# Kernel tuning notes

Hardware: AMD Instinct MI355X
Metric: run time of the kernel (lower is better)

Reference implementation:

```python
import jax, jax.numpy as jnp
import numpy as np

NUM_NODES = 100000
NODE_FEAT_DIM = 512
EDGE_FEAT_DIM = 512
MEM_DIM = NODE_FEAT_DIM + EDGE_FEAT_DIM  # 1024
BATCH = 65536


def setup_inputs() -> dict:
    key = jax.random.key(0)
    k_ids, k_mem, k_emb, kq, ks, kk = jax.random.split(key, 6)
    scale = 1.0 / np.sqrt(MEM_DIM)
    inp = {
        "node_ids": jax.random.randint(k_ids, (BATCH,), 0, NUM_NODES, dtype=jnp.int64)
        if jax.config.jax_enable_x64 else
        jax.random.randint(k_ids, (BATCH,), 0, NUM_NODES, dtype=jnp.int32),
        # memory bank: (N, 1, D); randomized (instead of the zero init) so math is non-trivial
        "node_memories": jax.random.normal(k_mem, (NUM_NODES, 1, MEM_DIM), dtype=jnp.float32) * 0.02,
        "node_embedding": jax.random.normal(k_emb, (NUM_NODES, MEM_DIM), dtype=jnp.float32) * 0.02,
        "Wq": jax.random.normal(jax.random.fold_in(kq, 0), (MEM_DIM, NODE_FEAT_DIM), dtype=jnp.float32) * scale,
        "bq": jnp.zeros((NODE_FEAT_DIM,), dtype=jnp.float32),
        "Ws": jax.random.normal(jax.random.fold_in(ks, 0), (MEM_DIM, NODE_FEAT_DIM), dtype=jnp.float32) * scale,
        "bs": jnp.zeros((NODE_FEAT_DIM,), dtype=jnp.float32),
        "Wk": jax.random.normal(jax.random.fold_in(kk, 0), (MEM_DIM, NODE_FEAT_DIM), dtype=jnp.float32) * scale,
        "bk": jnp.zeros((NODE_FEAT_DIM,), dtype=jnp.float32),
    }
    return inp


def reference(node_ids, node_memories, node_embedding, Wq, bq, Ws, bs, Wk, bk):
    ids = node_ids.astype(jnp.int32)
    # torch.sum(node_memories[ids], dim=2): reduces feature dim -> (B, 1)
    mem_sum = jnp.sum(node_memories[ids], axis=2)          # (B, 1)
    x = mem_sum + node_embedding[ids]                      # broadcast -> (B, D)
    q = jax.nn.sigmoid(x @ Wq + bq)                        # (B, node_feat_dim)
    s = jax.nn.sigmoid(x @ Ws + bs)
    k = jax.nn.sigmoid(x @ Wk + bk)
    return (q, s, k)
```

## Files before the change

kernel.cpp:

```cpp
#include <hip/hip_runtime.h>
#include <hip/hip_bf16.h>
#include <stdint.h>

#define BATCH_N 65536
#define KDIM 1024
#define NTOT 1536

typedef __bf16 bf16x8 __attribute__((ext_vector_type(8)));
typedef float f32x4 __attribute__((ext_vector_type(4)));

__device__ __forceinline__ unsigned short f2bf(float f) {
    unsigned u = __builtin_bit_cast(unsigned, f);
    u += 0x7FFFu + ((u >> 16) & 1u);
    return (unsigned short)(u >> 16);
}

__global__ __launch_bounds__(256) void prep_kernel(
    const int* __restrict__ ids,
    const float* __restrict__ mem,
    const float* __restrict__ emb,
    unsigned short* __restrict__ x)
{
    const int b = blockIdx.x;
    const int t = threadIdx.x;
    const int id = ids[b];
    const float4* m4 = (const float4*)(mem + (size_t)id * KDIM);
    const float4* e4 = (const float4*)(emb + (size_t)id * KDIM);
    float4 v = m4[t];
    float s = v.x + v.y + v.z + v.w;
    #pragma unroll
    for (int off = 32; off >= 1; off >>= 1) s += __shfl_down(s, off, 64);
    __shared__ float wsum[4];
    const int lane = t & 63, w = t >> 6;
    if (lane == 0) wsum[w] = s;
    __syncthreads();
    const float tot = wsum[0] + wsum[1] + wsum[2] + wsum[3];
    float4 e = e4[t];
    ushort4 o;
    o.x = f2bf(tot + e.x);
    o.y = f2bf(tot + e.y);
    o.z = f2bf(tot + e.z);
    o.w = f2bf(tot + e.w);
    const int k   = t * 4;
    const int ksw = k ^ ((b & 7) << 3);
    *(ushort4*)(x + (size_t)b * KDIM + ksw) = o;
}

__global__ __launch_bounds__(256) void wconv_kernel(
    const float* __restrict__ Wq, const float* __restrict__ Ws,
    const float* __restrict__ Wk, unsigned short* __restrict__ wt)
{
    const int gt = blockIdx.x * 256 + threadIdx.x;
    const int n  = gt % NTOT;
    const int kb = (gt / NTOT) * 4;
    const float* W = (n < 512) ? Wq : ((n < 1024) ? Ws : Wk);
    const int nn = n & 511;
    ushort4 o;
    o.x = f2bf(W[(size_t)(kb + 0) * 512 + nn]);
    o.y = f2bf(W[(size_t)(kb + 1) * 512 + nn]);
    o.z = f2bf(W[(size_t)(kb + 2) * 512 + nn]);
    o.w = f2bf(W[(size_t)(kb + 3) * 512 + nn]);
    const int ksw = kb ^ ((n & 7) << 3);
    *(ushort4*)(wt + (size_t)n * KDIM + ksw) = o;
}

#define BM 128
#define BN 128
#define BK 64
#define MT 512
#define NT 12
#define NWG (MT * NT)

__global__ __launch_bounds__(256, 2) void gemm_kernel(
    const unsigned short* __restrict__ X,
    const unsigned short* __restrict__ Wt,
    const float* __restrict__ bq, const float* __restrict__ bs,
    const float* __restrict__ bk, float* __restrict__ out)
{
    __shared__ __align__(16) unsigned short lA[BM * BK];
    __shared__ __align__(16) unsigned short lB[BN * BK];

    const int tid  = threadIdx.x;
    const int xcd  = blockIdx.x & 7;
    const int idx  = blockIdx.x >> 3;
    const int wgid = xcd * (NWG / 8) + idx;
    const int nt   = wgid % NT;
    const int mt   = wgid / NT;
    const int m0   = mt * BM;
    const int n0   = nt * BN;
    const int wid  = tid >> 6;
    const int lane = tid & 63;
    const int wr   = wid >> 1, wc = wid & 1;

    f32x4 acc[4][4];
    #pragma unroll
    for (int i = 0; i < 4; i++)
        #pragma unroll
        for (int j = 0; j < 4; j++)
            acc[i][j] = f32x4{0.f, 0.f, 0.f, 0.f};

    const unsigned short* gA = X  + (size_t)(m0 + (tid >> 3)) * KDIM + (size_t)(tid & 7) * 8;
    const unsigned short* gB = Wt + (size_t)(n0 + (tid >> 3)) * KDIM + (size_t)(tid & 7) * 8;

    for (int ks = 0; ks < KDIM; ks += BK) {
        __syncthreads();
        #pragma unroll
        for (int i = 0; i < 4; i++) {
            __builtin_amdgcn_global_load_lds(
                (const __attribute__((address_space(1))) void*)(gA + (size_t)i * 32 * KDIM + ks),
                (__attribute__((address_space(3))) void*)(&lA[(i * 256 + (tid & 192)) * 8]),
                16, 0, 0);
        }
        #pragma unroll
        for (int i = 0; i < 4; i++) {
            __builtin_amdgcn_global_load_lds(
                (const __attribute__((address_space(1))) void*)(gB + (size_t)i * 32 * KDIM + ks),
                (__attribute__((address_space(3))) void*)(&lB[(i * 256 + (tid & 192)) * 8]),
                16, 0, 0);
        }
        __syncthreads();

        #pragma unroll
        for (int kk = 0; kk < 2; kk++) {
            const int r16  = lane & 15;
            const int kbyt = ((lane >> 4) << 4) + kk * 64;
            const int kswz = kbyt ^ ((r16 & 7) << 4);
            bf16x8 af[4], bfr[4];
            #pragma unroll
            for (int i = 0; i < 4; i++) {
                const int row = wr * 64 + i * 16 + r16;
                af[i] = *(const bf16x8*)((const char*)lA + row * 128 + kswz);
            }
            #pragma unroll
            for (int j = 0; j < 4; j++) {
                const int row = wc * 64 + j * 16 + r16;
                bfr[j] = *(const bf16x8*)((const char*)lB + row * 128 + kswz);
            }
            #pragma unroll
            for (int i = 0; i < 4; i++)
                #pragma unroll
                for (int j = 0; j < 4; j++)
                    acc[i][j] = __builtin_amdgcn_mfma_f32_16x16x32_bf16(
                        af[i], bfr[j], acc[i][j], 0, 0, 0);
        }
    }

    const float* bias = (n0 < 512) ? bq : ((n0 < 1024) ? bs : bk);
    float* obase = out + (size_t)(n0 >> 9) * ((size_t)BATCH_N * 512);
    const int nb = n0 & 511;
    #pragma unroll
    for (int j = 0; j < 4; j++) {
        const int col = nb + wc * 64 + j * 16 + (lane & 15);
        const float bv = bias[col];
        #pragma unroll
        for (int i = 0; i < 4; i++) {
            const int rbase = m0 + wr * 64 + i * 16 + ((lane >> 4) << 2);
            #pragma unroll
            for (int r = 0; r < 4; r++) {
                float v = acc[i][j][r] + bv;
                v = 1.0f / (1.0f + __expf(-v));
                __builtin_nontemporal_store(v, &obase[(size_t)(rbase + r) * 512 + col]);
            }
        }
    }
}

extern "C" void kernel_launch(void* const* d_in, const int* in_sizes, int n_in,
                              void* d_out, int out_size, void* d_ws, size_t ws_size,
                              hipStream_t stream) {
    const int*   ids = (const int*)d_in[0];
    const float* mem = (const float*)d_in[1];
    const float* emb = (const float*)d_in[2];
    const float* Wq  = (const float*)d_in[3];
    const float* bq  = (const float*)d_in[4];
    const float* Ws  = (const float*)d_in[5];
    const float* bs  = (const float*)d_in[6];
    const float* Wk  = (const float*)d_in[7];
    const float* bk  = (const float*)d_in[8];
    float* out = (float*)d_out;

    unsigned short* x  = (unsigned short*)d_ws;
    unsigned short* wt = x + (size_t)BATCH_N * KDIM;

    hipLaunchKernelGGL(wconv_kernel, dim3(NTOT), dim3(256), 0, stream, Wq, Ws, Wk, wt);
    hipLaunchKernelGGL(prep_kernel, dim3(BATCH_N), dim3(256), 0, stream, ids, mem, emb, x);
    hipLaunchKernelGGL(gemm_kernel, dim3(NWG), dim3(256), 0, stream,
                       x, wt, bq, bs, bk, out);
}
```

Before: 415.3 us.

## Triple-buffer GEMM LDS with 512-thread 128x256 tiles and interleaved prefetch

Makes the GEMM tile 128x256 and the workgroup 512 threads in a 2x4 wave grid, so each A tile is reused across twice as many output columns. It adds a three-stage LDS ring filled with global_load_lds, issuing the prefetch of tile k+2 in the same phases that run MFMAs on tile k. It uses raw s_barrier and vmcnt waits plus s_setprio around the MFMA blocks, aiming to hide global-load latency behind compute. LDS use rises to 144 KB per block, which likely allows only one block per CU despite the launch bound, and the hand-placed waitcnts are easy to get wrong.

Measured after the change: 468.9 us. 12.9% more time.

```diff
diff --git a/kernel.cpp b/kernel.cpp
--- a/kernel.cpp
+++ b/kernel.cpp
@@ -65,20 +65,22 @@
 }
 
 #define BM 128
-#define BN 128
+#define BN 256
 #define BK 64
-#define MT 512
-#define NT 12
+#define MT (BATCH_N / BM)
+#define NT (NTOT / BN)
 #define NWG (MT * NT)
 
-__global__ __launch_bounds__(256, 2) void gemm_kernel(
+#define BAR() asm volatile("s_barrier" ::: "memory")
+
+__global__ __launch_bounds__(512, 2) void gemm_kernel(
     const unsigned short* __restrict__ X,
     const unsigned short* __restrict__ Wt,
     const float* __restrict__ bq, const float* __restrict__ bs,
     const float* __restrict__ bk, float* __restrict__ out)
 {
-    __shared__ __align__(16) unsigned short lA[BM * BK];
-    __shared__ __align__(16) unsigned short lB[BN * BK];
+    __shared__ __align__(16) unsigned short sA[3][BM * BK];
+    __shared__ __align__(16) unsigned short sB[3][BN * BK];
 
     const int tid  = threadIdx.x;
     const int xcd  = blockIdx.x & 7;
@@ -90,7 +92,11 @@
     const int n0   = nt * BN;
     const int wid  = tid >> 6;
     const int lane = tid & 63;
-    const int wr   = wid >> 1, wc = wid & 1;
+    const int wm   = wid >> 2;
+    const int wn   = wid & 3;
+    const int r16  = lane & 15;
+    const int kb0  = (lane >> 4) << 4;
+    const int ksw  = (r16 & 7) << 4;
 
     f32x4 acc[4][4];
     #pragma unroll
@@ -99,62 +105,74 @@
         for (int j = 0; j < 4; j++)
             acc[i][j] = f32x4{0.f, 0.f, 0.f, 0.f};
 
-    const unsigned short* gA = X  + (size_t)(m0 + (tid >> 3)) * KDIM + (size_t)(tid & 7) * 8;
-    const unsigned short* gB = Wt + (size_t)(n0 + (tid >> 3)) * KDIM + (size_t)(tid & 7) * 8;
-
-    for (int ks = 0; ks < KDIM; ks += BK) {
-        __syncthreads();
-        #pragma unroll
-        for (int i = 0; i < 4; i++) {
-            __builtin_amdgcn_global_load_lds(
-                (const __attribute__((address_space(1))) void*)(gA + (size_t)i * 32 * KDIM + ks),
-                (__attribute__((address_space(3))) void*)(&lA[(i * 256 + (tid & 192)) * 8]),
-                16, 0, 0);
-        }
-        #pragma unroll
-        for (int i = 0; i < 4; i++) {
-            __builtin_amdgcn_global_load_lds(
-                (const __attribute__((address_space(1))) void*)(gB + (size_t)i * 32 * KDIM + ks),
-                (__attribute__((address_space(3))) void*)(&lB[(i * 256 + (tid & 192)) * 8]),
-                16, 0, 0);
-        }
-        __syncthreads();
-
-        #pragma unroll
-        for (int kk = 0; kk < 2; kk++) {
-            const int r16  = lane & 15;
-            const int kbyt = ((lane >> 4) << 4) + kk * 64;
-            const int kswz = kbyt ^ ((r16 & 7) << 4);
-            bf16x8 af[4], bfr[4];
-            #pragma unroll
-            for (int i = 0; i < 4; i++) {
-                const int row = wr * 64 + i * 16 + r16;
-                af[i] = *(const bf16x8*)((const char*)lA + row * 128 + kswz);
-            }
-            #pragma unroll
-            for (int j = 0; j < 4; j++) {
-                const int row = wc * 64 + j * 16 + r16;
-                bfr[j] = *(const bf16x8*)((const char*)lB + row * 128 + kswz);
-            }
-            #pragma unroll
-            for (int i = 0; i < 4; i++)
-                #pragma unroll
-                for (int j = 0; j < 4; j++)
-                    acc[i][j] = __builtin_amdgcn_mfma_f32_16x16x32_bf16(
-                        af[i], bfr[j], acc[i][j], 0, 0, 0);
-        }
+    const unsigned short* gA = X  + (size_t)(m0 + (tid >> 3)) * KDIM + (tid & 7) * 8;
+    const unsigned short* gB = Wt + (size_t)(n0 + (tid >> 3)) * KDIM + (tid & 7) * 8;
+    const int ldst = (tid & 448) * 8;
+
+#define STA(buf, kt, c) __builtin_amdgcn_global_load_lds( \
+    (const __attribute__((address_space(1))) void*)(gA + (size_t)(c) * 64 * KDIM + (kt) * BK), \
+    (__attribute__((address_space(3))) void*)(&sA[buf][(c) * 4096 + ldst]), 16, 0, 0)
+#define STB(buf, kt, c) __builtin_amdgcn_global_load_lds( \
+    (const __attribute__((address_space(1))) void*)(gB + (size_t)(c) * 64 * KDIM + (kt) * BK), \
+    (__attribute__((address_space(3))) void*)(&sB[buf][(c) * 4096 + ldst]), 16, 0, 0)
+
+#define PHASE(rb, kkc, STAGE_STMTS, VMW) do {                                   \
+    const char* pa = (const char*)&sA[rb][0];                                    \
+    const char* pb = (const char*)&sB[rb][0];                                    \
+    bf16x8 af[4], bfr[4];                                                        \
+    _Pragma("unroll")                                                            \
+    for (int i = 0; i < 4; i++)                                                  \
+        af[i] = *(const bf16x8*)(pa + (wm * 64 + i * 16 + r16) * 128             \
+                                    + ((kb0 + (kkc) * 64) ^ ksw));               \
+    _Pragma("unroll")                                                            \
+    for (int j = 0; j < 4; j++)                                                  \
+        bfr[j] = *(const bf16x8*)(pb + (wn * 64 + j * 16 + r16) * 128            \
+                                     + ((kb0 + (kkc) * 64) ^ ksw));              \
+    STAGE_STMTS;                                                                 \
+    BAR();                                                                       \
+    asm volatile("s_waitcnt lgkmcnt(0)" ::: "memory");                           \
+    __builtin_amdgcn_s_setprio(1);                                               \
+    _Pragma("unroll")                                                            \
+    for (int i = 0; i < 4; i++)                                                  \
+        _Pragma("unroll")                                                        \
+        for (int j = 0; j < 4; j++)                                              \
+            acc[i][j] = __builtin_amdgcn_mfma_f32_16x16x32_bf16(                 \
+                af[i], bfr[j], acc[i][j], 0, 0, 0);                              \
+    __builtin_amdgcn_s_setprio(0);                                               \
+    VMW;                                                                         \
+    BAR();                                                                       \
+} while (0)
+
+    STA(0, 0, 0); STA(0, 0, 1); STB(0, 0, 0); STB(0, 0, 1); STB(0, 0, 2); STB(0, 0, 3);
+    STA(1, 1, 0); STA(1, 1, 1); STB(1, 1, 0); STB(1, 1, 1); STB(1, 1, 2); STB(1, 1, 3);
+    asm volatile("s_waitcnt vmcnt(6)" ::: "memory");
+    BAR();
+
+    int rb = 0, wb = 2;
+    for (int k = 0; k < 14; ++k) {
+        const int kt = k + 2;
+        PHASE(rb, 0, ({ STA(wb, kt, 0); STA(wb, kt, 1); STB(wb, kt, 0); }), (void)0);
+        PHASE(rb, 1, ({ STB(wb, kt, 1); STB(wb, kt, 2); STB(wb, kt, 3); }),
+              asm volatile("s_waitcnt vmcnt(6)" ::: "memory"));
+        rb = (rb == 2) ? 0 : rb + 1;
+        wb = (wb == 2) ? 0 : wb + 1;
     }
-
-    const float* bias = (n0 < 512) ? bq : ((n0 < 1024) ? bs : bk);
-    float* obase = out + (size_t)(n0 >> 9) * ((size_t)BATCH_N * 512);
-    const int nb = n0 & 511;
+    PHASE(rb, 0, (void)0, (void)0);
+    PHASE(rb, 1, (void)0, asm volatile("s_waitcnt vmcnt(0)" ::: "memory"));
+    rb = (rb == 2) ? 0 : rb + 1;
+    PHASE(rb, 0, (void)0, (void)0);
+    PHASE(rb, 1, (void)0, (void)0);
+
+    const int grp = nt >> 1;
+    const float* bias = (grp == 0) ? bq : ((grp == 1) ? bs : bk);
+    float* obase = out + (size_t)grp * ((size_t)BATCH_N * 512);
     #pragma unroll
     for (int j = 0; j < 4; j++) {
-        const int col = nb + wc * 64 + j * 16 + (lane & 15);
+        const int col = (nt & 1) * 256 + wn * 64 + j * 16 + r16;
         const float bv = bias[col];
         #pragma unroll
         for (int i = 0; i < 4; i++) {
-            const int rbase = m0 + wr * 64 + i * 16 + ((lane >> 4) << 2);
+            const int rbase = m0 + wm * 64 + i * 16 + ((lane >> 4) << 2);
             #pragma unroll
             for (int r = 0; r < 4; r++) {
                 float v = acc[i][j][r] + bv;
@@ -163,6 +181,9 @@
             }
         }
     }
+#undef STA
+#undef STB
+#undef PHASE
 }
 
 extern "C" void kernel_launch(void* const* d_in, const int* in_sizes, int n_in,
@@ -184,6 +205,6 @@
 
     hipLaunchKernelGGL(wconv_kernel, dim3(NTOT), dim3(256), 0, stream, Wq, Ws, Wk, wt);
     hipLaunchKernelGGL(prep_kernel, dim3(BATCH_N), dim3(256), 0, stream, ids, mem, emb, x);
-    hipLaunchKernelGGL(gemm_kernel, dim3(NWG), dim3(256), 0, stream,
+    hipLaunchKernelGGL(gemm_kernel, dim3(NWG), dim3(512), 0, stream,
                        x, wt, bq, bs, bk, out);
 }
```
